# Optimization experiments

Hardware: AMD Instinct MI355X
Metric: run time of the kernel (lower is better)

Reference implementation:

```python
import jax, jax.numpy as jnp
import numpy as np

B, C, H, W = 8, 256, 64, 64
IC = C // 2  # inter_channel


def setup_inputs() -> dict:
    key = jax.random.key(0)
    k0, k1, k2, k3, k4 = jax.random.split(key, 5)
    s = 0.05
    return {
        "x": jax.random.normal(k0, (B, C, H, W), dtype=jnp.float32),
        "w_theta": jax.random.normal(k1, (IC, C), dtype=jnp.float32) * s,
        "w_phi": jax.random.normal(k2, (IC, C), dtype=jnp.float32) * s,
        "w_g": jax.random.normal(k3, (IC, C), dtype=jnp.float32) * s,
        "w_mask": jax.random.normal(k4, (C, IC), dtype=jnp.float32) * s,
    }


def reference(x, w_theta, w_phi, w_g, w_mask):
    b, c, h, w = x.shape
    ic = c // 2
    # 1x1 convs (bias=False) == channel-mixing einsums -> (b, ic, h, w)
    theta = jnp.einsum("oc,bchw->bohw", w_theta, x)
    phi = jnp.einsum("oc,bchw->bohw", w_phi, x)
    g = jnp.einsum("oc,bchw->bohw", w_g, x)
    # Faithful to original: .view(b, c, -1) on a (b, ic, h, w) tensor
    # => sequence length N = h*w/2, feature dim = c (full channels).
    n = ic * h * w // c  # = h*w/2
    x_theta = theta.reshape(b, c, n).transpose(0, 2, 1)  # (b, n, c)
    x_phi = phi.reshape(b, c, n)                          # (b, c, n)
    x_g = g.reshape(b, c, n).transpose(0, 2, 1)           # (b, n, c)
    attn = jnp.matmul(x_theta, x_phi)                     # (b, n, n)
    # Original uses nn.Softmax(dim=1): normalize over ROWS, not last axis.
    attn = jax.nn.softmax(attn, axis=1)
    out = jnp.matmul(attn, x_g)                           # (b, n, c)
    out = out.transpose(0, 2, 1).reshape(b, ic, h, w)     # (b, ic, h, w)
    mask = jnp.einsum("oc,bchw->bohw", w_mask, out)       # (b, c, h, w)
    return mask + x
```

## Files before the change

kernel.cpp:

```cpp
#include <hip/hip_runtime.h>

typedef __attribute__((ext_vector_type(8))) __bf16 bf16x8;
typedef __attribute__((ext_vector_type(4))) float f32x4;

#define LOG2E 1.4426950408889634f

#define XT_OFF   0ul
#define OTA_OFF  0ul
#define TT_OFF   16777216ul
#define PT_OFF   25165824ul
#define G_OFF    33554432ul
#define W3_OFF   41943040ul
#define WM_OFF   42139648ul
#define ID_OFF   42205184ul
#define PART_OFF 42270720ul
#define WS_NEED  43319296ul

__device__ __forceinline__ void gload16(const __bf16* g, __bf16* l){
  __builtin_amdgcn_global_load_lds((const __attribute__((address_space(1))) void*)g,
                                   (__attribute__((address_space(3))) void*)l, 16, 0, 0);
}

__global__ __launch_bounds__(256) void k_weights(const float* wt, const float* wp,
                                                 const float* wg, const float* wm,
                                                 __bf16* W3, __bf16* Wm){
  int idx = blockIdx.x*256 + threadIdx.x;
  if (idx < 98304){
    float v = (idx < 32768) ? wt[idx] : (idx < 65536) ? wp[idx - 32768] : wg[idx - 65536];
    W3[idx] = (__bf16)v;
  } else if (idx < 131072){
    Wm[idx - 98304] = (__bf16)wm[idx - 98304];
  }
}

__global__ __launch_bounds__(256) void k_xt(const float* x, __bf16* Xt){
  __shared__ float tile[64][65];
  int b = blockIdx.z, c0 = blockIdx.y*64, p0 = blockIdx.x*64;
  int t = threadIdx.x, col = t & 63, r0 = t >> 6;
  const float* xb = x + ((size_t)b*256 + c0)*4096 + p0;
  #pragma unroll
  for (int rr = 0; rr < 16; ++rr){
    int row = rr*4 + r0;
    tile[row][col] = xb[(size_t)row*4096 + col];
  }
  __syncthreads();
  __bf16* xo = Xt + ((size_t)b*4096 + p0)*256 + c0;
  #pragma unroll
  for (int rr = 0; rr < 16; ++rr){
    int prow = rr*4 + r0;
    xo[(size_t)prow*256 + col] = (__bf16)tile[col][prow];
  }
}

__global__ __launch_bounds__(256) void k_conv3(const __bf16* Xt, const __bf16* W3,
                                               __bf16* Tt, __bf16* Pt, __bf16* G){
  __shared__ __bf16 As[128*72];
  __shared__ __bf16 Bs[64*72];
  int b = blockIdx.z, p0 = blockIdx.x*128, o0 = blockIdx.y*64;
  int tid = threadIdx.x, lane = tid & 63, wave = tid >> 6;
  int wm = wave >> 1, wn = wave & 1;
  f32x4 acc[4][2] = {};
  const __bf16* Ab = Xt + ((size_t)b*4096 + p0)*256;
  const __bf16* Bb = W3 + (size_t)o0*256;
  for (int kc = 0; kc < 4; ++kc){
    int k0 = kc*64;
    #pragma unroll
    for (int it = 0; it < 4; ++it){
      int s = tid + it*256, row = s >> 3, sk = s & 7;
      *(uint4*)&As[row*72 + sk*8] = *(const uint4*)(Ab + (size_t)row*256 + k0 + sk*8);
    }
    #pragma unroll
    for (int it = 0; it < 2; ++it){
      int s = tid + it*256, row = s >> 3, sk = s & 7;
      *(uint4*)&Bs[row*72 + sk*8] = *(const uint4*)(Bb + (size_t)row*256 + k0 + sk*8);
    }
    __syncthreads();
    #pragma unroll
    for (int ks = 0; ks < 2; ++ks){
      int koff = ks*32 + (lane>>4)*8;
      bf16x8 af[4], bfr[2];
      #pragma unroll
      for (int fm = 0; fm < 4; ++fm)
        af[fm] = *(const bf16x8*)&As[(wm*64 + fm*16 + (lane&15))*72 + koff];
      #pragma unroll
      for (int fn = 0; fn < 2; ++fn)
        bfr[fn] = *(const bf16x8*)&Bs[(wn*32 + fn*16 + (lane&15))*72 + koff];
      #pragma unroll
      for (int fm = 0; fm < 4; ++fm)
        #pragma unroll
        for (int fn = 0; fn < 2; ++fn)
          acc[fm][fn] = __builtin_amdgcn_mfma_f32_16x16x32_bf16(af[fm], bfr[fn], acc[fm][fn], 0, 0, 0);
    }
    __syncthreads();
  }
  #pragma unroll
  for (int fm = 0; fm < 4; ++fm)
    #pragma unroll
    for (int fn = 0; fn < 2; ++fn)
      #pragma unroll
      for (int r = 0; r < 4; ++r){
        int p = p0 + wm*64 + fm*16 + (lane>>4)*4 + r;
        int o = o0 + wn*32 + fn*16 + (lane&15);
        __bf16 v = (__bf16)acc[fm][fn][r];
        int i = p & 2047, ph = p >> 11;
        if (o < 128)      Tt[((size_t)b*2048 + i)*256 + 2*o + ph] = v;
        else if (o < 256) Pt[((size_t)b*2048 + i)*256 + 2*(o-128) + ph] = v;
        else              G [((size_t)b*256 + 2*(o-256) + ph)*2048 + i] = v;
      }
}

__global__ __launch_bounds__(256) void k_sexp(const __bf16* Tt, const __bf16* Pt,
                                              __bf16* S, float* PART, int js0){
  __shared__ __bf16 As[128*64];
  __shared__ __bf16 Bs[128*64];
  int bid = blockIdx.x;
  int b = bid & 7, r2 = bid >> 3;
  int m = r2 & 15, n = r2 >> 4;
  int m0 = m*128;
  int tid = threadIdx.x, lane = tid & 63, w = tid >> 6;
  int lr = lane & 15, kq = lane >> 4;
  int wm = w >> 1, wn = w & 1;
  const __bf16* Ab = Tt + ((size_t)b*2048 + m0)*256;
  const __bf16* Bb = Pt + ((size_t)b*2048 + js0 + n*128)*256;
  int laneRow = lane >> 3;
  int laneSw  = ((lane & 7) ^ laneRow) * 8;
  const __bf16* ga = Ab + (size_t)laneRow*256 + laneSw;
  const __bf16* gb = Bb + (size_t)laneRow*256 + laneSw;
  f32x4 acc[4][4] = {};
  for (int kc = 0; kc < 4; ++kc){
    int k0 = kc*64;
    #pragma unroll
    for (int u = 0; u < 4; ++u){
      int c = w*4 + u;
      gload16(ga + (size_t)c*8*256 + k0, &As[c*512]);
      gload16(gb + (size_t)c*8*256 + k0, &Bs[c*512]);
    }
    __syncthreads();
    #pragma unroll
    for (int ks = 0; ks < 2; ++ks){
      bf16x8 af[4], bf[4];
      #pragma unroll
      for (int fm = 0; fm < 4; ++fm){
        int ar = wm*64 + fm*16 + lr;
        af[fm] = *(const bf16x8*)&As[ar*64 + (((ks*4 + kq) ^ (ar & 7))*8)];
      }
      #pragma unroll
      for (int fn = 0; fn < 4; ++fn){
        int br = wn*64 + fn*16 + lr;
        bf[fn] = *(const bf16x8*)&Bs[br*64 + (((ks*4 + kq) ^ (br & 7))*8)];
      }
      #pragma unroll
      for (int fm = 0; fm < 4; ++fm)
        #pragma unroll
        for (int fn = 0; fn < 4; ++fn)
          acc[fm][fn] = __builtin_amdgcn_mfma_f32_16x16x32_bf16(af[fm], bf[fn], acc[fm][fn], 0, 0, 0);
    }
    __syncthreads();
  }
  __bf16* Sb = S + ((size_t)b*2048 + m0)*1024 + n*128;
  #pragma unroll
  for (int fn = 0; fn < 4; ++fn){
    int jc = wn*64 + fn*16 + lr;
    float v = 0.f;
    #pragma unroll
    for (int fm = 0; fm < 4; ++fm){
      int ib = wm*64 + fm*16 + kq*4;
      #pragma unroll
      for (int r = 0; r < 4; ++r){
        float e = exp2f(acc[fm][fn][r] * LOG2E);
        v += e;
        Sb[(size_t)(ib + r)*1024 + jc] = (__bf16)e;
      }
    }
    v += __shfl_xor(v, 16);
    v += __shfl_xor(v, 32);
    if (kq == 0)
      PART[((size_t)b*32 + m*2 + wm)*1024 + n*128 + jc] = v;
  }
}

__global__ __launch_bounds__(256) void k_invd(const float* PART, float* invD, int js0){
  int bid = blockIdx.x;
  int b = bid & 7, seg = bid >> 3;
  int jl = seg*256 + threadIdx.x;
  float s = 0.f;
  #pragma unroll
  for (int it = 0; it < 32; ++it) s += PART[((size_t)b*32 + it)*1024 + jl];
  invD[(size_t)b*2048 + js0 + jl] = 1.0f / s;
}

__global__ __launch_bounds__(256) void k_gscale(__bf16* G, const float* invD, int js0){
  int bid = blockIdx.x;
  int b = bid >> 8, c = bid & 255;
  int jl = threadIdx.x * 4;
  __bf16* gp = G + ((size_t)b*256 + c)*2048 + js0 + jl;
  const float* dp = invD + (size_t)b*2048 + js0 + jl;
  f32x4 d = *(const f32x4*)dp;
  __bf16 gv[4];
  *(uint2*)gv = *(const uint2*)gp;
  #pragma unroll
  for (int e = 0; e < 4; ++e) gv[e] = (__bf16)((float)gv[e] * d[e]);
  *(uint2*)gp = *(const uint2*)gv;
}

__global__ __launch_bounds__(256) void k_pv(const __bf16* S, const __bf16* G,
                                            float* OTacc, int js0, int first){
  __shared__ __bf16 As[128*64];
  __shared__ __bf16 Bs[64*64];
  int bid = blockIdx.x;
  int b = bid & 7, r2 = bid >> 3;
  int m = r2 & 15, n = r2 >> 4;
  int m0 = m*128, n0 = n*64;
  int tid = threadIdx.x, lane = tid & 63, w = tid >> 6;
  int lr = lane & 15, kq = lane >> 4;
  int wm = w >> 1, wn = w & 1;
  const __bf16* Ab = S + ((size_t)b*2048 + m0)*1024;
  const __bf16* Bb = G + ((size_t)b*256 + n0)*2048 + js0;
  int laneRow = lane >> 3;
  int laneSw  = ((lane & 7) ^ laneRow) * 8;
  const __bf16* ga = Ab + (size_t)laneRow*1024 + laneSw;
  const __bf16* gb = Bb + (size_t)laneRow*2048 + laneSw;
  f32x4 acc[4][2] = {};
  for (int kc = 0; kc < 16; ++kc){
    int k0 = kc*64;
    #pragma unroll
    for (int u = 0; u < 4; ++u){
      int c = w*4 + u;
      gload16(ga + (size_t)c*8*1024 + k0, &As[c*512]);
    }
    #pragma unroll
    for (int u = 0; u < 2; ++u){
      int c = w*2 + u;
      gload16(gb + (size_t)c*8*2048 + k0, &Bs[c*512]);
    }
    __syncthreads();
    #pragma unroll
    for (int ks = 0; ks < 2; ++ks){
      bf16x8 af[4], bf[2];
      #pragma unroll
      for (int fm = 0; fm < 4; ++fm){
        int ar = wm*64 + fm*16 + lr;
        af[fm] = *(const bf16x8*)&As[ar*64 + (((ks*4 + kq) ^ (ar & 7))*8)];
      }
      #pragma unroll
      for (int fn = 0; fn < 2; ++fn){
        int br = wn*32 + fn*16 + lr;
        bf[fn] = *(const bf16x8*)&Bs[br*64 + (((ks*4 + kq) ^ (br & 7))*8)];
      }
      #pragma unroll
      for (int fm = 0; fm < 4; ++fm)
        #pragma unroll
        for (int fn = 0; fn < 2; ++fn)
          acc[fm][fn] = __builtin_amdgcn_mfma_f32_16x16x32_bf16(af[fm], bf[fn], acc[fm][fn], 0, 0, 0);
    }
    __syncthreads();
  }
  float* Ob = OTacc + (size_t)b*4096*128;
  if (first){
    #pragma unroll
    for (int fm = 0; fm < 4; ++fm)
      #pragma unroll
      for (int fn = 0; fn < 2; ++fn)
        #pragma unroll
        for (int r = 0; r < 4; ++r){
          int i = m0 + wm*64 + fm*16 + kq*4 + r;
          int c = n0 + wn*32 + fn*16 + lr;
          Ob[(size_t)(((c & 1) << 11) + i)*128 + (c >> 1)] = acc[fm][fn][r];
        }
  } else {
    #pragma unroll
    for (int fm = 0; fm < 4; ++fm)
      #pragma unroll
      for (int fn = 0; fn < 2; ++fn)
        #pragma unroll
        for (int r = 0; r < 4; ++r){
          int i = m0 + wm*64 + fm*16 + kq*4 + r;
          int c = n0 + wn*32 + fn*16 + lr;
          size_t idx = (size_t)(((c & 1) << 11) + i)*128 + (c >> 1);
          Ob[idx] += acc[fm][fn][r];
        }
  }
}

__global__ __launch_bounds__(256) void k_mask(const float* OTacc, const __bf16* Wm,
                                              const float* x, float* out){
  __shared__ __bf16 As[128*72];
  __shared__ __bf16 Bs[64*72];
  int b = blockIdx.z, p0 = blockIdx.x*128, o0 = blockIdx.y*64;
  int tid = threadIdx.x, lane = tid & 63, wave = tid >> 6;
  int wm = wave >> 1, wn = wave & 1;
  f32x4 acc[4][2] = {};
  const float* Ab = OTacc + ((size_t)b*4096 + p0)*128;
  const __bf16* Bb = Wm + (size_t)o0*128;
  for (int kc = 0; kc < 2; ++kc){
    int k0 = kc*64;
    #pragma unroll
    for (int it = 0; it < 8; ++it){
      int idx = it*256 + tid;
      int row = idx >> 4, c4 = (idx & 15)*4;
      f32x4 vv = *(const f32x4*)(Ab + (size_t)row*128 + k0 + c4);
      __bf16 tmp[4];
      #pragma unroll
      for (int e = 0; e < 4; ++e) tmp[e] = (__bf16)vv[e];
      *(uint2*)&As[row*72 + c4] = *(const uint2*)tmp;
    }
    #pragma unroll
    for (int itc = 0; itc < 2; ++itc){
      int s = tid + itc*256, row = s >> 3, sk = s & 7;
      *(uint4*)&Bs[row*72 + sk*8] = *(const uint4*)(Bb + (size_t)row*128 + k0 + sk*8);
    }
    __syncthreads();
    #pragma unroll
    for (int ks = 0; ks < 2; ++ks){
      int koff = ks*32 + (lane>>4)*8;
      bf16x8 af[4], bfr[2];
      #pragma unroll
      for (int fm = 0; fm < 4; ++fm)
        af[fm] = *(const bf16x8*)&As[(wm*64 + fm*16 + (lane&15))*72 + koff];
      #pragma unroll
      for (int fn = 0; fn < 2; ++fn)
        bfr[fn] = *(const bf16x8*)&Bs[(wn*32 + fn*16 + (lane&15))*72 + koff];
      #pragma unroll
      for (int fm = 0; fm < 4; ++fm)
        #pragma unroll
        for (int fn = 0; fn < 2; ++fn)
          acc[fm][fn] = __builtin_amdgcn_mfma_f32_16x16x32_bf16(af[fm], bfr[fn], acc[fm][fn], 0, 0, 0);
    }
    __syncthreads();
  }
  #pragma unroll
  for (int fm = 0; fm < 4; ++fm)
    #pragma unroll
    for (int fn = 0; fn < 2; ++fn){
      int pb = p0 + wm*64 + fm*16 + (lane>>4)*4;
      int o = o0 + wn*32 + fn*16 + (lane&15);
      size_t idx = ((size_t)b*256 + o)*4096 + pb;
      f32x4 xv = *(const f32x4*)(x + idx);
      f32x4 ov = acc[fm][fn] + xv;
      *(f32x4*)(out + idx) = ov;
    }
}

extern "C" void kernel_launch(void* const* d_in, const int* in_sizes, int n_in,
                              void* d_out, int out_size, void* d_ws, size_t ws_size,
                              hipStream_t stream){
  if (ws_size < WS_NEED) return;
  const float* x  = (const float*)d_in[0];
  const float* wt = (const float*)d_in[1];
  const float* wp = (const float*)d_in[2];
  const float* wg = (const float*)d_in[3];
  const float* wm = (const float*)d_in[4];
  char* ws = (char*)d_ws;
  __bf16* Xt   = (__bf16*)(ws + XT_OFF);
  float* OTacc = (float*)(ws + OTA_OFF);
  __bf16* Tt   = (__bf16*)(ws + TT_OFF);
  __bf16* Pt   = (__bf16*)(ws + PT_OFF);
  __bf16* G    = (__bf16*)(ws + G_OFF);
  __bf16* W3   = (__bf16*)(ws + W3_OFF);
  __bf16* Wm   = (__bf16*)(ws + WM_OFF);
  float* invD  = (float*)(ws + ID_OFF);
  float* PART  = (float*)(ws + PART_OFF);
  __bf16* S    = (__bf16*)d_out;
  float* out   = (float*)d_out;

  k_weights<<<512, 256, 0, stream>>>(wt, wp, wg, wm, W3, Wm);
  k_xt<<<dim3(64, 4, 8), 256, 0, stream>>>(x, Xt);
  k_conv3<<<dim3(32, 6, 8), 256, 0, stream>>>(Xt, W3, Tt, Pt, G);
  for (int s = 0; s < 2; ++s){
    int js0 = s * 1024;
    k_sexp<<<1024, 256, 0, stream>>>(Tt, Pt, S, PART, js0);
    k_invd<<<32, 256, 0, stream>>>(PART, invD, js0);
    k_gscale<<<2048, 256, 0, stream>>>(G, invD, js0);
    k_pv<<<512, 256, 0, stream>>>(S, G, OTacc, js0, s == 0 ? 1 : 0);
  }
  k_mask<<<dim3(32, 4, 8), 256, 0, stream>>>(OTacc, Wm, x, out);
}
```

Measured before the change: 156.1 us.

## Double-buffer LDS loads in score and PV GEMMs, stage exp tile through LDS

Both the score-exp and PV kernels now prefetch the next K chunk into a second LDS buffer while MFMAs run on the current one, with an explicit vmcnt wait and a single barrier per iteration. The intent is to hide global-to-LDS load latency behind compute. The score kernel also writes its exp tile into padded LDS and then stores it to global memory as coalesced 16-byte vectors instead of scattered 2-byte writes. PV block ordering is changed so that blocks sharing the same S rows are adjacent, which should improve L2 reuse. The cost is double the LDS footprint per block (64KB for the score kernel), which may lower occupancy.

```diff
diff --git a/kernel.cpp b/kernel.cpp
--- a/kernel.cpp
+++ b/kernel.cpp
@@ -111,8 +111,7 @@
 
 __global__ __launch_bounds__(256) void k_sexp(const __bf16* Tt, const __bf16* Pt,
                                               __bf16* S, float* PART, int js0){
-  __shared__ __bf16 As[128*64];
-  __shared__ __bf16 Bs[128*64];
+  __shared__ __bf16 smem[4][128*64];
   int bid = blockIdx.x;
   int b = bid & 7, r2 = bid >> 3;
   int m = r2 & 15, n = r2 >> 4;
@@ -127,15 +126,27 @@
   const __bf16* ga = Ab + (size_t)laneRow*256 + laneSw;
   const __bf16* gb = Bb + (size_t)laneRow*256 + laneSw;
   f32x4 acc[4][4] = {};
+  #pragma unroll
+  for (int u = 0; u < 4; ++u){
+    int c = w*4 + u;
+    gload16(ga + (size_t)c*8*256, &smem[0][c*512]);
+    gload16(gb + (size_t)c*8*256, &smem[1][c*512]);
+  }
+  asm volatile("s_waitcnt vmcnt(0)" ::: "memory");
+  __syncthreads();
   for (int kc = 0; kc < 4; ++kc){
-    int k0 = kc*64;
-    #pragma unroll
-    for (int u = 0; u < 4; ++u){
-      int c = w*4 + u;
-      gload16(ga + (size_t)c*8*256 + k0, &As[c*512]);
-      gload16(gb + (size_t)c*8*256 + k0, &Bs[c*512]);
-    }
-    __syncthreads();
+    int cur = kc & 1;
+    if (kc < 3){
+      int k0 = (kc + 1)*64;
+      #pragma unroll
+      for (int u = 0; u < 4; ++u){
+        int c = w*4 + u;
+        gload16(ga + (size_t)c*8*256 + k0, &smem[(cur^1)*2][c*512]);
+        gload16(gb + (size_t)c*8*256 + k0, &smem[(cur^1)*2+1][c*512]);
+      }
+    }
+    const __bf16* As = smem[cur*2];
+    const __bf16* Bs = smem[cur*2+1];
     #pragma unroll
     for (int ks = 0; ks < 2; ++ks){
       bf16x8 af[4], bf[4];
@@ -155,9 +166,13 @@
         for (int fn = 0; fn < 4; ++fn)
           acc[fm][fn] = __builtin_amdgcn_mfma_f32_16x16x32_bf16(af[fm], bf[fn], acc[fm][fn], 0, 0, 0);
     }
-    __syncthreads();
-  }
-  __bf16* Sb = S + ((size_t)b*2048 + m0)*1024 + n*128;
+    if (kc < 3){
+      asm volatile("s_waitcnt vmcnt(0)" ::: "memory");
+      __syncthreads();
+    }
+  }
+  __syncthreads();
+  __bf16* eL = (__bf16*)smem;
   #pragma unroll
   for (int fn = 0; fn < 4; ++fn){
     int jc = wn*64 + fn*16 + lr;
@@ -169,13 +184,21 @@
       for (int r = 0; r < 4; ++r){
         float e = exp2f(acc[fm][fn][r] * LOG2E);
         v += e;
-        Sb[(size_t)(ib + r)*1024 + jc] = (__bf16)e;
+        eL[(ib + r)*136 + jc] = (__bf16)e;
       }
     }
     v += __shfl_xor(v, 16);
     v += __shfl_xor(v, 32);
     if (kq == 0)
       PART[((size_t)b*32 + m*2 + wm)*1024 + n*128 + jc] = v;
+  }
+  __syncthreads();
+  __bf16* Sb = S + ((size_t)b*2048 + m0)*1024 + n*128;
+  #pragma unroll
+  for (int u = 0; u < 8; ++u){
+    int idx = u*256 + tid;
+    int row = idx >> 4, ch = idx & 15;
+    *(uint4*)(Sb + (size_t)row*1024 + ch*8) = *(const uint4*)&eL[row*136 + ch*8];
   }
 }
 
@@ -205,11 +228,11 @@
 
 __global__ __launch_bounds__(256) void k_pv(const __bf16* S, const __bf16* G,
                                             float* OTacc, int js0, int first){
-  __shared__ __bf16 As[128*64];
-  __shared__ __bf16 Bs[64*64];
+  __shared__ __bf16 sA[2][128*64];
+  __shared__ __bf16 sB[2][64*64];
   int bid = blockIdx.x;
   int b = bid & 7, r2 = bid >> 3;
-  int m = r2 & 15, n = r2 >> 4;
+  int n = r2 & 3, m = r2 >> 2;
   int m0 = m*128, n0 = n*64;
   int tid = threadIdx.x, lane = tid & 63, w = tid >> 6;
   int lr = lane & 15, kq = lane >> 4;
@@ -221,19 +244,35 @@
   const __bf16* ga = Ab + (size_t)laneRow*1024 + laneSw;
   const __bf16* gb = Bb + (size_t)laneRow*2048 + laneSw;
   f32x4 acc[4][2] = {};
+  #pragma unroll
+  for (int u = 0; u < 4; ++u){
+    int c = w*4 + u;
+    gload16(ga + (size_t)c*8*1024, &sA[0][c*512]);
+  }
+  #pragma unroll
+  for (int u = 0; u < 2; ++u){
+    int c = w*2 + u;
+    gload16(gb + (size_t)c*8*2048, &sB[0][c*512]);
+  }
+  asm volatile("s_waitcnt vmcnt(0)" ::: "memory");
+  __syncthreads();
   for (int kc = 0; kc < 16; ++kc){
-    int k0 = kc*64;
-    #pragma unroll
-    for (int u = 0; u < 4; ++u){
-      int c = w*4 + u;
-      gload16(ga + (size_t)c*8*1024 + k0, &As[c*512]);
-    }
-    #pragma unroll
-    for (int u = 0; u < 2; ++u){
-      int c = w*2 + u;
-      gload16(gb + (size_t)c*8*2048 + k0, &Bs[c*512]);
-    }
-    __syncthreads();
+    int cur = kc & 1;
+    if (kc < 15){
+      int k0 = (kc + 1)*64;
+      #pragma unroll
+      for (int u = 0; u < 4; ++u){
+        int c = w*4 + u;
+        gload16(ga + (size_t)c*8*1024 + k0, &sA[cur^1][c*512]);
+      }
+      #pragma unroll
+      for (int u = 0; u < 2; ++u){
+        int c = w*2 + u;
+        gload16(gb + (size_t)c*8*2048 + k0, &sB[cur^1][c*512]);
+      }
+    }
+    const __bf16* As = sA[cur];
+    const __bf16* Bs = sB[cur];
     #pragma unroll
     for (int ks = 0; ks < 2; ++ks){
       bf16x8 af[4], bf[2];
@@ -253,7 +292,10 @@
         for (int fn = 0; fn < 2; ++fn)
           acc[fm][fn] = __builtin_amdgcn_mfma_f32_16x16x32_bf16(af[fm], bf[fn], acc[fm][fn], 0, 0, 0);
     }
-    __syncthreads();
+    if (kc < 15){
+      asm volatile("s_waitcnt vmcnt(0)" ::: "memory");
+      __syncthreads();
+    }
   }
   float* Ob = OTacc + (size_t)b*4096*128;
   if (first){
```

After: 158.5 us. No clear change (+1.5%).

## Restructure score GEMM with resident A tile and triple-buffered pipelined loads

Applied to the files above, without the earlier changes.

k_sexp now runs 512-thread blocks that keep a 64x256 Tt tile resident in LDS. They loop over 8 column chunks, streaming Pt through a triple-buffered LDS ring with loads issued two steps ahead, and write exp outputs through an LDS staging buffer as coalesced 16-byte stores. k_pv gets the same triple-buffered prefetch pipeline with partial vmcnt waits and a reordered block index (n fastest) so neighbouring blocks share S rows. PART grows to 64 partial rows per batch and k_invd reads all of them. This is meant to hide global-load latency and cut redundant Tt reads, at the cost of fewer, larger blocks and more LDS per block.

```diff
diff --git a/kernel.cpp b/kernel.cpp
--- a/kernel.cpp
+++ b/kernel.cpp
@@ -14,7 +14,7 @@
 #define WM_OFF   42139648ul
 #define ID_OFF   42205184ul
 #define PART_OFF 42270720ul
-#define WS_NEED  43319296ul
+#define WS_NEED  44367872ul
 
 __device__ __forceinline__ void gload16(const __bf16* g, __bf16* l){
   __builtin_amdgcn_global_load_lds((const __attribute__((address_space(1))) void*)g,
@@ -109,73 +109,102 @@
       }
 }
 
-__global__ __launch_bounds__(256) void k_sexp(const __bf16* Tt, const __bf16* Pt,
+__global__ __launch_bounds__(512) void k_sexp(const __bf16* Tt, const __bf16* Pt,
                                               __bf16* S, float* PART, int js0){
-  __shared__ __bf16 As[128*64];
-  __shared__ __bf16 Bs[128*64];
+  __shared__ __bf16 As[64*256];
+  __shared__ __bf16 Bs[3][128*64];
+  __shared__ __bf16 eL[64*136];
   int bid = blockIdx.x;
-  int b = bid & 7, r2 = bid >> 3;
-  int m = r2 & 15, n = r2 >> 4;
-  int m0 = m*128;
+  int b = bid & 7, m = bid >> 3, m0 = m*64;
   int tid = threadIdx.x, lane = tid & 63, w = tid >> 6;
   int lr = lane & 15, kq = lane >> 4;
-  int wm = w >> 1, wn = w & 1;
+  int iw = w >> 2, jw = w & 3;
   const __bf16* Ab = Tt + ((size_t)b*2048 + m0)*256;
-  const __bf16* Bb = Pt + ((size_t)b*2048 + js0 + n*128)*256;
-  int laneRow = lane >> 3;
-  int laneSw  = ((lane & 7) ^ laneRow) * 8;
-  const __bf16* ga = Ab + (size_t)laneRow*256 + laneSw;
-  const __bf16* gb = Bb + (size_t)laneRow*256 + laneSw;
-  f32x4 acc[4][4] = {};
-  for (int kc = 0; kc < 4; ++kc){
-    int k0 = kc*64;
-    #pragma unroll
-    for (int u = 0; u < 4; ++u){
-      int c = w*4 + u;
-      gload16(ga + (size_t)c*8*256 + k0, &As[c*512]);
-      gload16(gb + (size_t)c*8*256 + k0, &Bs[c*512]);
-    }
-    __syncthreads();
-    #pragma unroll
-    for (int ks = 0; ks < 2; ++ks){
-      bf16x8 af[4], bf[4];
-      #pragma unroll
-      for (int fm = 0; fm < 4; ++fm){
-        int ar = wm*64 + fm*16 + lr;
-        af[fm] = *(const bf16x8*)&As[ar*64 + (((ks*4 + kq) ^ (ar & 7))*8)];
-      }
-      #pragma unroll
-      for (int fn = 0; fn < 4; ++fn){
-        int br = wn*64 + fn*16 + lr;
-        bf[fn] = *(const bf16x8*)&Bs[br*64 + (((ks*4 + kq) ^ (br & 7))*8)];
-      }
-      #pragma unroll
-      for (int fm = 0; fm < 4; ++fm)
-        #pragma unroll
-        for (int fn = 0; fn < 4; ++fn)
-          acc[fm][fn] = __builtin_amdgcn_mfma_f32_16x16x32_bf16(af[fm], bf[fn], acc[fm][fn], 0, 0, 0);
-    }
-    __syncthreads();
-  }
-  __bf16* Sb = S + ((size_t)b*2048 + m0)*1024 + n*128;
-  #pragma unroll
-  for (int fn = 0; fn < 4; ++fn){
-    int jc = wn*64 + fn*16 + lr;
-    float v = 0.f;
-    #pragma unroll
-    for (int fm = 0; fm < 4; ++fm){
-      int ib = wm*64 + fm*16 + kq*4;
-      #pragma unroll
-      for (int r = 0; r < 4; ++r){
-        float e = exp2f(acc[fm][fn][r] * LOG2E);
-        v += e;
-        Sb[(size_t)(ib + r)*1024 + jc] = (__bf16)e;
-      }
-    }
-    v += __shfl_xor(v, 16);
-    v += __shfl_xor(v, 32);
-    if (kq == 0)
-      PART[((size_t)b*32 + m*2 + wm)*1024 + n*128 + jc] = v;
+  const __bf16* Pb = Pt + ((size_t)b*2048 + js0)*256;
+  __bf16* Sb = S + ((size_t)b*2048 + m0)*1024;
+  int aRow = lane >> 5, aSlot = lane & 31;
+  int bRow = lane >> 3, bSlot = lane & 7;
+  #pragma unroll
+  for (int u = 0; u < 4; ++u){
+    int r0 = u*16 + w*2 + aRow;
+    gload16(Ab + (size_t)r0*256 + ((aSlot ^ (r0 & 7))*8), &As[u*4096 + w*512]);
+  }
+  #pragma unroll
+  for (int t0 = 0; t0 < 2; ++t0){
+    #pragma unroll
+    for (int u = 0; u < 2; ++u){
+      int row = u*64 + w*8 + bRow;
+      gload16(Pb + (size_t)(0*128 + row)*256 + t0*64 + ((bSlot ^ (row & 7))*8),
+              &Bs[t0][u*4096 + w*512]);
+    }
+  }
+  for (int n = 0; n < 8; ++n){
+    f32x4 acc[2][2] = {};
+    #pragma unroll
+    for (int kc = 0; kc < 4; ++kc){
+      int t = n*4 + kc;
+      if (t == 31) asm volatile("s_waitcnt vmcnt(0)" ::: "memory");
+      else         asm volatile("s_waitcnt vmcnt(2)" ::: "memory");
+      __builtin_amdgcn_s_barrier();
+      if (t + 2 < 32){
+        int t2 = t + 2, n2 = t2 >> 2, kc2 = t2 & 3, bf2 = t2 % 3;
+        #pragma unroll
+        for (int u = 0; u < 2; ++u){
+          int row = u*64 + w*8 + bRow;
+          gload16(Pb + (size_t)(n2*128 + row)*256 + kc2*64 + ((bSlot ^ (row & 7))*8),
+                  &Bs[bf2][u*4096 + w*512]);
+        }
+      }
+      const __bf16* Bc = &Bs[t % 3][0];
+      #pragma unroll
+      for (int ks = 0; ks < 2; ++ks){
+        int slotA = kc*8 + ks*4 + kq;
+        int slotB = ks*4 + kq;
+        bf16x8 af[2], bf[2];
+        #pragma unroll
+        for (int fm = 0; fm < 2; ++fm){
+          int ar = iw*32 + fm*16 + lr;
+          af[fm] = *(const bf16x8*)&As[ar*256 + ((slotA ^ (ar & 7))*8)];
+        }
+        #pragma unroll
+        for (int fn = 0; fn < 2; ++fn){
+          int br = jw*32 + fn*16 + lr;
+          bf[fn] = *(const bf16x8*)&Bc[br*64 + ((slotB ^ (br & 7))*8)];
+        }
+        #pragma unroll
+        for (int fm = 0; fm < 2; ++fm)
+          #pragma unroll
+          for (int fn = 0; fn < 2; ++fn)
+            acc[fm][fn] = __builtin_amdgcn_mfma_f32_16x16x32_bf16(af[fm], bf[fn], acc[fm][fn], 0, 0, 0);
+      }
+    }
+    #pragma unroll
+    for (int fn = 0; fn < 2; ++fn){
+      int jc = jw*32 + fn*16 + lr;
+      float v = 0.f;
+      #pragma unroll
+      for (int fm = 0; fm < 2; ++fm){
+        int ib = iw*32 + fm*16 + kq*4;
+        #pragma unroll
+        for (int r = 0; r < 4; ++r){
+          float e = exp2f(acc[fm][fn][r] * LOG2E);
+          v += e;
+          eL[(ib + r)*136 + jc] = (__bf16)e;
+        }
+      }
+      v += __shfl_xor(v, 16);
+      v += __shfl_xor(v, 32);
+      if (kq == 0)
+        PART[((size_t)b*64 + m*2 + iw)*1024 + n*128 + jc] = v;
+    }
+    asm volatile("s_waitcnt lgkmcnt(0)" ::: "memory");
+    __builtin_amdgcn_s_barrier();
+    #pragma unroll
+    for (int u2 = 0; u2 < 2; ++u2){
+      int idx = u2*512 + tid;
+      int row = idx >> 4, sl = idx & 15;
+      *(uint4*)(Sb + (size_t)row*1024 + n*128 + sl*8) = *(const uint4*)&eL[row*136 + sl*8];
+    }
   }
 }
 
@@ -185,7 +214,7 @@
   int jl = seg*256 + threadIdx.x;
   float s = 0.f;
   #pragma unroll
-  for (int it = 0; it < 32; ++it) s += PART[((size_t)b*32 + it)*1024 + jl];
+  for (int it = 0; it < 64; ++it) s += PART[((size_t)b*64 + it)*1024 + jl];
   invD[(size_t)b*2048 + js0 + jl] = 1.0f / s;
 }
 
@@ -205,47 +234,68 @@
 
 __global__ __launch_bounds__(256) void k_pv(const __bf16* S, const __bf16* G,
                                             float* OTacc, int js0, int first){
-  __shared__ __bf16 As[128*64];
-  __shared__ __bf16 Bs[64*64];
+  __shared__ __bf16 sA[3][128*64];
+  __shared__ __bf16 sB[3][64*64];
   int bid = blockIdx.x;
   int b = bid & 7, r2 = bid >> 3;
-  int m = r2 & 15, n = r2 >> 4;
+  int n = r2 & 3, m = r2 >> 2;
   int m0 = m*128, n0 = n*64;
   int tid = threadIdx.x, lane = tid & 63, w = tid >> 6;
   int lr = lane & 15, kq = lane >> 4;
   int wm = w >> 1, wn = w & 1;
   const __bf16* Ab = S + ((size_t)b*2048 + m0)*1024;
   const __bf16* Bb = G + ((size_t)b*256 + n0)*2048 + js0;
-  int laneRow = lane >> 3;
-  int laneSw  = ((lane & 7) ^ laneRow) * 8;
-  const __bf16* ga = Ab + (size_t)laneRow*1024 + laneSw;
-  const __bf16* gb = Bb + (size_t)laneRow*2048 + laneSw;
+  int bRow = lane >> 3, bSlot = lane & 7;
   f32x4 acc[4][2] = {};
-  for (int kc = 0; kc < 16; ++kc){
-    int k0 = kc*64;
+  #pragma unroll
+  for (int t0 = 0; t0 < 2; ++t0){
     #pragma unroll
     for (int u = 0; u < 4; ++u){
-      int c = w*4 + u;
-      gload16(ga + (size_t)c*8*1024 + k0, &As[c*512]);
+      int row = u*32 + w*8 + bRow;
+      gload16(Ab + (size_t)row*1024 + t0*64 + ((bSlot ^ (row & 7))*8),
+              &sA[t0][u*2048 + w*512]);
     }
     #pragma unroll
     for (int u = 0; u < 2; ++u){
-      int c = w*2 + u;
-      gload16(gb + (size_t)c*8*2048 + k0, &Bs[c*512]);
-    }
-    __syncthreads();
+      int row = u*32 + w*8 + bRow;
+      gload16(Bb + (size_t)row*2048 + t0*64 + ((bSlot ^ (row & 7))*8),
+              &sB[t0][u*2048 + w*512]);
+    }
+  }
+  for (int t = 0; t < 16; ++t){
+    if (t == 15) asm volatile("s_waitcnt vmcnt(0)" ::: "memory");
+    else         asm volatile("s_waitcnt vmcnt(6)" ::: "memory");
+    __builtin_amdgcn_s_barrier();
+    if (t + 2 < 16){
+      int t2 = t + 2, bf2 = t2 % 3, k0 = t2*64;
+      #pragma unroll
+      for (int u = 0; u < 4; ++u){
+        int row = u*32 + w*8 + bRow;
+        gload16(Ab + (size_t)row*1024 + k0 + ((bSlot ^ (row & 7))*8),
+                &sA[bf2][u*2048 + w*512]);
+      }
+      #pragma unroll
+      for (int u = 0; u < 2; ++u){
+        int row = u*32 + w*8 + bRow;
+        gload16(Bb + (size_t)row*2048 + k0 + ((bSlot ^ (row & 7))*8),
+                &sB[bf2][u*2048 + w*512]);
+      }
+    }
+    const __bf16* Ac = &sA[t % 3][0];
+    const __bf16* Bc = &sB[t % 3][0];
     #pragma unroll
     for (int ks = 0; ks < 2; ++ks){
+      int slot = ks*4 + kq;
       bf16x8 af[4], bf[2];
       #pragma unroll
       for (int fm = 0; fm < 4; ++fm){
         int ar = wm*64 + fm*16 + lr;
-        af[fm] = *(const bf16x8*)&As[ar*64 + (((ks*4 + kq) ^ (ar & 7))*8)];
+        af[fm] = *(const bf16x8*)&Ac[ar*64 + ((slot ^ (ar & 7))*8)];
       }
       #pragma unroll
       for (int fn = 0; fn < 2; ++fn){
         int br = wn*32 + fn*16 + lr;
-        bf[fn] = *(const bf16x8*)&Bs[br*64 + (((ks*4 + kq) ^ (br & 7))*8)];
+        bf[fn] = *(const bf16x8*)&Bc[br*64 + ((slot ^ (br & 7))*8)];
       }
       #pragma unroll
       for (int fm = 0; fm < 4; ++fm)
@@ -253,7 +303,6 @@
         for (int fn = 0; fn < 2; ++fn)
           acc[fm][fn] = __builtin_amdgcn_mfma_f32_16x16x32_bf16(af[fm], bf[fn], acc[fm][fn], 0, 0, 0);
     }
-    __syncthreads();
   }
   float* Ob = OTacc + (size_t)b*4096*128;
   if (first){
@@ -368,7 +417,7 @@
   k_conv3<<<dim3(32, 6, 8), 256, 0, stream>>>(Xt, W3, Tt, Pt, G);
   for (int s = 0; s < 2; ++s){
     int js0 = s * 1024;
-    k_sexp<<<1024, 256, 0, stream>>>(Tt, Pt, S, PART, js0);
+    k_sexp<<<256, 512, 0, stream>>>(Tt, Pt, S, PART, js0);
     k_invd<<<32, 256, 0, stream>>>(PART, invD, js0);
     k_gscale<<<2048, 256, 0, stream>>>(G, invD, js0);
     k_pv<<<512, 256, 0, stream>>>(S, G, OTacc, js0, s == 0 ? 1 : 0);
```

Result: slower. 173.9 us (+11.4%).
